# Kernel tuning notes

Hardware: AMD Instinct MI355X
Metric: run time of the kernel (lower is better)

Reference implementation:

```python
import jax, jax.numpy as jnp
import numpy as np

B, L, DM = 16, 1024, 128
DK = DV = 32
HF, HG, HC, HP, HT, HA = 2, 2, 2, 2, 1, 2  # full, log, local, prob, FFT, auto heads
MA = 25          # series_decomp moving average window
WIN = 32         # local attention causal window
EPS = 1e-5
SCALE = float(1.0 / np.sqrt(DK))

_i = np.arange(L)[:, None]
_j = np.arange(L)[None, :]
_d = _i - _j
# log-sparse: attend to self and keys at power-of-two causal distances
LOG_MASK = jnp.asarray((_d == 0) | ((_d > 0) & ((_d & (_d - 1)) == 0)))
LOC_MASK = jnp.asarray((_d >= 0) & (_d < WIN))
# ProbSparse (Informer, factor=5): fixed sample indices, u = U_part
_U = min(int(5 * np.ceil(np.log(L))), L)
PROB_IDX = jnp.asarray(np.random.RandomState(0).randint(0, L, size=(L, _U)))
AUTO_K = int(np.log(L))  # AutoCorrelation factor=1


def _cconv(x, w, b, pad):
    # x [B,L,DM] -> conv over time in NCH layout; pad-left = causal (Conv pad=2 + Chomp1d(2))
    y = jax.lax.conv_general_dilated(x.swapaxes(1, 2), w, (1,), [(pad, 0)],
                                     dimension_numbers=('NCH', 'OIH', 'NCH'))
    return y + b[None, :, None]


def _heads(y, H, d):
    # faithful to torch: .view(B, L, H, d) applied to [B, C, L] conv output (memory reinterpret)
    return y.reshape(y.shape[0], L, H, d)


def _qkv(xq, xk, xv, wq, bq, wk, bk, wv, bv, H):
    Q = _heads(_cconv(xq, wq, bq, 2), H, DK)
    K = _heads(_cconv(xk, wk, bk, 2), H, DK)
    V = _heads(_cconv(xv, wv, bv, 0), H, DV)
    return Q, K, V


def _attn(Q, K, V, mask=None):
    s = jnp.einsum('blhe,bshe->bhls', Q, K) * SCALE
    if mask is not None:
        s = jnp.where(mask, s, -1e9)
    return jnp.einsum('bhls,bshd->blhd', jax.nn.softmax(s, axis=-1), V)


def _prob_attn(Q, K, V):
    q, k, v = Q.swapaxes(1, 2), K.swapaxes(1, 2), V.swapaxes(1, 2)  # [B,H,L,D]
    Ks = k[:, :, PROB_IDX]                                  # [B,H,L,U,D] sampled keys
    qk = jnp.einsum('bhld,bhlud->bhlu', q, Ks)
    M = qk.max(-1) - qk.sum(-1) / L                         # sparsity measure
    top = jax.lax.top_k(M, _U)[1]                           # [B,H,u] active queries
    qr = jnp.take_along_axis(q, top[..., None], axis=2)
    sc = jnp.einsum('bhud,bhsd->bhus', qr, k) * SCALE
    cu = jnp.einsum('bhus,bhsd->bhud', jax.nn.softmax(sc, -1), v)
    ctx = jnp.broadcast_to(v.mean(axis=2, keepdims=True), v.shape)  # lazy queries get mean(V)
    bi = jnp.arange(v.shape[0])[:, None, None]
    hi = jnp.arange(v.shape[1])[None, :, None]
    return ctx.at[bi, hi, top].set(cu).swapaxes(1, 2)


def _auto_corr(Q, K, V):
    q = Q.transpose(0, 2, 3, 1)  # [B,H,E,L]
    k = K.transpose(0, 2, 3, 1)
    v = V.transpose(0, 2, 3, 1)
    corr = jnp.fft.irfft(jnp.fft.rfft(q, axis=-1) * jnp.conj(jnp.fft.rfft(k, axis=-1)), n=L, axis=-1)
    mv = corr.mean(axis=1).mean(axis=1)                     # [B,L] mean over heads+channels
    idx = jax.lax.top_k(mv.mean(axis=0), AUTO_K)[1]         # shared top-k delays
    w = jax.nn.softmax(mv[:, idx], axis=-1)                 # [B,k]
    tt = jnp.arange(L)
    agg = jnp.zeros_like(v)
    for i in range(AUTO_K):
        agg = agg + v[..., (tt + idx[i]) % L] * w[:, i][:, None, None, None]
    return agg.transpose(0, 3, 1, 2)                        # [B,L,H,E]


def _mavg(x, k):
    # replicate-padded moving average (Autoformer series_decomp) via cumsum
    p = (k - 1) // 2
    xp = jnp.concatenate([jnp.repeat(x[:, :1], p, axis=1), x, jnp.repeat(x[:, -1:], p, axis=1)], axis=1)
    cs = jnp.cumsum(xp, axis=1)
    cs = jnp.concatenate([jnp.zeros_like(cs[:, :1]), cs], axis=1)
    return (cs[:, k:] - cs[:, :-k]) / k


def _forward(fl):
    (iq, ik, iv,
     wqf, bqf, wkf, bkf, wvf, bvf,
     wqg, bqg, wkg, bkg, wvg, bvg,
     wql, bql, wkl, bkl, wvl, bvl,
     wqp, bqp, wkp, bkp, wvp, bvp,
     wqa, bqa, wka, bka, wva, bva,
     wfft, bfft, wap, bap, was, bas, wfc) = fl
    ctx = []
    Q, K, V = _qkv(iq, ik, iv, wqf, bqf, wkf, bkf, wvf, bvf, HF)
    ctx.append(_attn(Q, K, V))
    Q, K, V = _qkv(iq, ik, iv, wqg, bqg, wkg, bkg, wvg, bvg, HG)
    ctx.append(_attn(Q, K, V, LOG_MASK))
    Q, K, V = _qkv(iq, ik, iv, wql, bql, wkl, bkl, wvl, bvl, HC)
    ctx.append(_attn(Q, K, V, LOC_MASK))
    Q, K, V = _qkv(iq, ik, iv, wqp, bqp, wkp, bkp, wvp, bvp, HP)
    ctx.append(_prob_attn(Q, K, V))
    cf = jnp.fft.fft(iq, axis=1).real                       # FFT branch
    ctx.append((cf @ wfft + bfft).reshape(B, L, HT, DV))
    Q, K, V = _qkv(iq, ik, iv, wqa, bqa, wka, bka, wva, bva, HA)
    ca = _auto_corr(Q, K, V).reshape(B, L, HA * DV) @ wap + bap
    ca = iq + ca                                            # residual (dropout=eval identity)
    ca = ca - _mavg(ca, MA)                                 # seasonal part of series_decomp
    ctx.append((ca @ was + bas).reshape(B, L, HA, DV))
    c = jnp.concatenate(ctx, axis=2).reshape(B, L, -1)
    out = c @ wfc + iq
    mu = out.mean(-1, keepdims=True)
    var = out.var(-1, keepdims=True)                        # fresh LayerNorm: weight=1, bias=0
    return (out - mu) / jnp.sqrt(var + EPS)


def setup_inputs() -> dict:
    ks = iter(jax.random.split(jax.random.key(0), 64))
    def n(shape, s=0.02):
        return jax.random.normal(next(ks), shape, dtype=jnp.float32) * s
    d = {}
    d['input_Q'] = jax.random.normal(next(ks), (B, L, DM), dtype=jnp.float32)
    d['input_K'] = jax.random.normal(next(ks), (B, L, DM), dtype=jnp.float32)
    d['input_V'] = jax.random.normal(next(ks), (B, L, DM), dtype=jnp.float32)
    for nm, H in [('full', HF), ('log', HG), ('loc', HC), ('prob', HP), ('auto', HA)]:
        d['wq_' + nm] = n((DK * H, DM, 3)); d['bq_' + nm] = n((DK * H,))
        d['wk_' + nm] = n((DK * H, DM, 3)); d['bk_' + nm] = n((DK * H,))
        d['wv_' + nm] = n((DV * H, DM, 1)); d['bv_' + nm] = n((DV * H,))
    d['w_fft'] = n((DM, DV * HT)); d['b_fft'] = n((DV * HT,))
    d['w_aproj'] = n((DV * HA, DM)); d['b_aproj'] = n((DM,))
    d['w_asize'] = n((DM, DV * HA)); d['b_asize'] = n((DV * HA,))
    d['w_fc'] = n(((HF + HG + HC + HP + HT + HA) * DV, DM))
    return d


def reference(input_Q, input_K, input_V, wq_full, bq_full, wk_full, bk_full, wv_full, bv_full, wq_log, bq_log, wk_log, bk_log, wv_log, bv_log, wq_loc, bq_loc, wk_loc, bk_loc, wv_loc, bv_loc, wq_prob, bq_prob, wk_prob, bk_prob, wv_prob, bv_prob, wq_auto, bq_auto, wk_auto, bk_auto, wv_auto, bv_auto, w_fft, b_fft, w_aproj, b_aproj, w_asize, b_asize, w_fc):
    return _forward((input_Q, input_K, input_V, wq_full, bq_full, wk_full, bk_full, wv_full, bv_full, wq_log, bq_log, wk_log, bk_log, wv_log, bv_log, wq_loc, bq_loc, wk_loc, bk_loc, wv_loc, bv_loc, wq_prob, bq_prob, wk_prob, bk_prob, wv_prob, bv_prob, wq_auto, bq_auto, wk_auto, bk_auto, wv_auto, bv_auto, w_fft, b_fft, w_aproj, b_aproj, w_asize, b_asize, w_fc))
```

## Files before the change

### kernel.cpp

```cpp
#include <hip/hip_runtime.h>
#include <hip/hip_bf16.h>
#include <math.h>

#define B_   16
#define L_   1024
#define SCALE_ 0.17677669529663687f

__global__ void mt_kernel(int* __restrict__ pidx) {
  __shared__ unsigned int mt[624];
  int tid = threadIdx.x;
  if (tid == 0) {
    unsigned int s = 0u;
    for (int i = 0; i < 624; ++i) {
      mt[i] = s;
      s = 1812433253u * (s ^ (s >> 30)) + (unsigned)(i + 1);
    }
  }
  __syncthreads();
  const unsigned int HI = 0x80000000u, LO = 0x7fffffffu, MM = 0x9908b0dfu;
  for (int blk = 0; blk < 58; ++blk) {
    unsigned int n0 = 0, n1 = 0, n2 = 0, old623 = 0;
    bool a0 = tid < 227, a2 = tid < 169;
    if (a0) {
      unsigned int y0 = (mt[tid] & HI) | (mt[tid + 1] & LO);
      n0 = mt[tid + 397] ^ (y0 >> 1) ^ ((y0 & 1u) ? MM : 0u);
      unsigned int y1 = (mt[tid + 227] & HI) | (mt[tid + 228] & LO);
      n1 = n0 ^ (y1 >> 1) ^ ((y1 & 1u) ? MM : 0u);
      if (a2) {
        unsigned int y2 = (mt[tid + 454] & HI) | (mt[tid + 455] & LO);
        n2 = n1 ^ (y2 >> 1) ^ ((y2 & 1u) ? MM : 0u);
      }
      if (tid == 169) old623 = mt[623];
    }
    __syncthreads();
    if (a0) {
      mt[tid] = n0;
      mt[tid + 227] = n1;
      if (a2) mt[tid + 454] = n2;
    }
    __syncthreads();
    if (tid == 169) {
      unsigned int y = (old623 & HI) | (mt[0] & LO);
      mt[623] = n1 ^ (y >> 1) ^ ((y & 1u) ? MM : 0u);
    }
    __syncthreads();
    for (int i = tid; i < 624; i += 256) {
      int g = blk * 624 + i;
      if (g < 35840) {
        unsigned int y = mt[i];
        y ^= y >> 11;
        y ^= (y << 7) & 0x9d2c5680u;
        y ^= (y << 15) & 0xefc60000u;
        y ^= y >> 18;
        pidx[g] = (int)(y & 1023u);
      }
    }
  }
}

__device__ __forceinline__ void conv_body(const float* __restrict__ x,
                                          const float* __restrict__ w,
                                          const float* __restrict__ bias,
                                          float* __restrict__ out,
                                          float* smem, int b, int t0, int tid, int is1) {
  int cp = tid & 31;
  int tg = tid >> 5;
  int tt0 = tg * 8;
  float acc0[8], acc1[8];
  float b0v = bias[cp], b1v = bias[cp + 32];
  #pragma unroll
  for (int j = 0; j < 8; ++j) { acc0[j] = b0v; acc1[j] = b1v; }
  if (!is1) {
    float* xs = smem;
    float* ws = smem + 8448;
    for (int i = tid; i < 66 * 128; i += 256) {
      int r = i >> 7, d = i & 127;
      int t = t0 - 2 + r;
      xs[r * 128 + d] = (t >= 0) ? x[(size_t)b * 131072 + (size_t)t * 128 + d] : 0.0f;
    }
    for (int dc = 0; dc < 128; dc += 16) {
      __syncthreads();
      {
        int row = tid >> 2, sub = tid & 3;
        const float* wsrc = w + row * 384 + dc * 3 + sub * 12;
        float* wdst = ws + row * 52 + sub * 12;
        #pragma unroll
        for (int k = 0; k < 12; ++k) wdst[k] = wsrc[k];
      }
      __syncthreads();
      #pragma unroll
      for (int dl = 0; dl < 16; dl += 4) {
        int d0 = dc + dl;
        float4 xr[10];
        #pragma unroll
        for (int r = 0; r < 10; ++r) xr[r] = *(const float4*)&xs[(tt0 + r) * 128 + d0];
        float4 wa0 = *(const float4*)&ws[cp * 52 + dl * 3];
        float4 wa1 = *(const float4*)&ws[cp * 52 + dl * 3 + 4];
        float4 wa2 = *(const float4*)&ws[cp * 52 + dl * 3 + 8];
        float4 wb0 = *(const float4*)&ws[(cp + 32) * 52 + dl * 3];
        float4 wb1 = *(const float4*)&ws[(cp + 32) * 52 + dl * 3 + 4];
        float4 wb2 = *(const float4*)&ws[(cp + 32) * 52 + dl * 3 + 8];
        float w0r[12] = {wa0.x, wa0.y, wa0.z, wa0.w, wa1.x, wa1.y, wa1.z, wa1.w,
                         wa2.x, wa2.y, wa2.z, wa2.w};
        float w1r[12] = {wb0.x, wb0.y, wb0.z, wb0.w, wb1.x, wb1.y, wb1.z, wb1.w,
                         wb2.x, wb2.y, wb2.z, wb2.w};
        #pragma unroll
        for (int j = 0; j < 8; ++j) {
          float a0 = acc0[j], a1 = acc1[j];
          #pragma unroll
          for (int k = 0; k < 3; ++k) {
            float4 xv = xr[j + k];
            a0 = fmaf(w0r[0 + k], xv.x, a0);
            a0 = fmaf(w0r[3 + k], xv.y, a0);
            a0 = fmaf(w0r[6 + k], xv.z, a0);
            a0 = fmaf(w0r[9 + k], xv.w, a0);
            a1 = fmaf(w1r[0 + k], xv.x, a1);
            a1 = fmaf(w1r[3 + k], xv.y, a1);
            a1 = fmaf(w1r[6 + k], xv.z, a1);
            a1 = fmaf(w1r[9 + k], xv.w, a1);
          }
          acc0[j] = a0; acc1[j] = a1;
        }
      }
    }
  } else {
    float* xs = smem;
    float* ws = smem + 8192;
    for (int i = tid; i < 64 * 128; i += 256) {
      int r = i >> 7, d = i & 127;
      xs[r * 128 + d] = x[(size_t)b * 131072 + (size_t)(t0 + r) * 128 + d];
    }
    for (int dc = 0; dc < 128; dc += 32) {
      __syncthreads();
      {
        int row = tid >> 2, sub = tid & 3;
        const float* wsrc = w + row * 128 + dc + sub * 8;
        float* wdst = ws + row * 36 + sub * 8;
        #pragma unroll
        for (int k = 0; k < 8; ++k) wdst[k] = wsrc[k];
      }
      __syncthreads();
      #pragma unroll
      for (int dl = 0; dl < 32; dl += 4) {
        int d0 = dc + dl;
        float4 wv0 = *(const float4*)&ws[cp * 36 + dl];
        float4 wv1 = *(const float4*)&ws[(cp + 32) * 36 + dl];
        #pragma unroll
        for (int j = 0; j < 8; ++j) {
          float4 xv = *(const float4*)&xs[(tt0 + j) * 128 + d0];
          float a0 = acc0[j], a1 = acc1[j];
          a0 = fmaf(wv0.x, xv.x, a0);
          a0 = fmaf(wv0.y, xv.y, a0);
          a0 = fmaf(wv0.z, xv.z, a0);
          a0 = fmaf(wv0.w, xv.w, a0);
          a1 = fmaf(wv1.x, xv.x, a1);
          a1 = fmaf(wv1.y, xv.y, a1);
          a1 = fmaf(wv1.z, xv.z, a1);
          a1 = fmaf(wv1.w, xv.w, a1);
          acc0[j] = a0; acc1[j] = a1;
        }
      }
    }
  }
  float* op0 = out + (size_t)b * 65536 + (size_t)cp * 1024 + t0 + tt0;
  float* op1 = out + (size_t)b * 65536 + (size_t)(cp + 32) * 1024 + t0 + tt0;
  *(float4*)op0 = make_float4(acc0[0], acc0[1], acc0[2], acc0[3]);
  *(float4*)(op0 + 4) = make_float4(acc0[4], acc0[5], acc0[6], acc0[7]);
  *(float4*)op1 = make_float4(acc1[0], acc1[1], acc1[2], acc1[3]);
  *(float4*)(op1 + 4) = make_float4(acc1[4], acc1[5], acc1[6], acc1[7]);
}

__global__ __launch_bounds__(256, 3)
void qkv_conv_kernel(const float* __restrict__ xq, const float* __restrict__ xk,
                     const float* __restrict__ xv,
                     const float* __restrict__ wq, const float* __restrict__ bq,
                     const float* __restrict__ wk, const float* __restrict__ bk,
                     const float* __restrict__ wv, const float* __restrict__ bv,
                     float* __restrict__ qo, float* __restrict__ ko,
                     float* __restrict__ vo) {
  __shared__ float smem[11776];
  int which = blockIdx.z;
  const float* x = (which == 0) ? xq : (which == 1) ? xk : xv;
  const float* w = (which == 0) ? wq : (which == 1) ? wk : wv;
  const float* bias = (which == 0) ? bq : (which == 1) ? bk : bv;
  float* out = (which == 0) ? qo : (which == 1) ? ko : vo;
  conv_body(x, w, bias, out, smem, blockIdx.y, blockIdx.x * 64, threadIdx.x, which == 2);
}

struct ConvArgs {
  const float* x[3];
  const float* w[15];
  const float* bia[15];
  float* outbase;
};
__global__ __launch_bounds__(256, 3)
void qkv_conv_all(ConvArgs a) {
  __shared__ float smem[11776];
  int z = blockIdx.z;
  int which = z % 3;
  float* out = a.outbase + (size_t)z * 1048576;
  conv_body(a.x[which], a.w[z], a.bia[z], out, smem, blockIdx.y, blockIdx.x * 64,
            threadIdx.x, which == 2);
}

__global__ __launch_bounds__(256, 2)
void attn_full_part(const float* __restrict__ Q, const float* __restrict__ K,
                    const float* __restrict__ V, float* __restrict__ part,
                    int stile, int nstage) {
  __shared__ float Ks[128][32];
  __shared__ float Vs[128][32];
  int bh = blockIdx.z, b = bh >> 1, h = bh & 1;
  int l = blockIdx.x * 256 + threadIdx.x;
  int s0 = blockIdx.y * stile;
  const float* Kb = K + (size_t)b * 65536 + h * 32;
  const float* Vb = V + (size_t)b * 65536 + h * 32;
  const float* Qb = Q + (size_t)b * 65536 + h * 32 + (size_t)l * 64;
  float q[32];
  #pragma unroll
  for (int i = 0; i < 8; ++i) {
    float4 v4 = ((const float4*)Qb)[i];
    q[4*i] = v4.x; q[4*i+1] = v4.y; q[4*i+2] = v4.z; q[4*i+3] = v4.w;
  }
  float o[32];
  #pragma unroll
  for (int d = 0; d < 32; ++d) o[d] = 0.0f;
  float ssum = 0.0f;
  for (int st = 0; st < nstage; ++st) {
    __syncthreads();
    int sb = s0 + st * 128;
    for (int i = threadIdx.x; i < 1024; i += 256) {
      int r = i >> 3, d4 = i & 7;
      ((float4*)&Ks[r][0])[d4] = *(const float4*)(Kb + (size_t)(sb + r) * 64 + d4 * 4);
      ((float4*)&Vs[r][0])[d4] = *(const float4*)(Vb + (size_t)(sb + r) * 64 + d4 * 4);
    }
    __syncthreads();
    for (int s = 0; s < 128; s += 2) {
      const float4* kp0 = (const float4*)&Ks[s][0];
      const float4* kp1 = (const float4*)&Ks[s + 1][0];
      float a0 = 0, a1 = 0, a2 = 0, a3 = 0;
      float c0 = 0, c1 = 0, c2 = 0, c3 = 0;
      #pragma unroll
      for (int i = 0; i < 8; ++i) {
        float4 k0 = kp0[i], k1 = kp1[i];
        float qx = q[4*i], qy = q[4*i+1], qz = q[4*i+2], qw = q[4*i+3];
        a0 = fmaf(qx, k0.x, a0); a1 = fmaf(qy, k0.y, a1);
        a2 = fmaf(qz, k0.z, a2); a3 = fmaf(qw, k0.w, a3);
        c0 = fmaf(qx, k1.x, c0); c1 = fmaf(qy, k1.y, c1);
        c2 = fmaf(qz, k1.z, c2); c3 = fmaf(qw, k1.w, c3);
      }
      float p0 = __expf(((a0 + a1) + (a2 + a3)) * SCALE_);
      float p1 = __expf(((c0 + c1) + (c2 + c3)) * SCALE_);
      ssum += p0 + p1;
      const float4* vp0 = (const float4*)&Vs[s][0];
      const float4* vp1 = (const float4*)&Vs[s + 1][0];
      #pragma unroll
      for (int i = 0; i < 8; ++i) {
        float4 v0 = vp0[i], v1 = vp1[i];
        o[4*i]   = fmaf(p0, v0.x, fmaf(p1, v1.x, o[4*i]));
        o[4*i+1] = fmaf(p0, v0.y, fmaf(p1, v1.y, o[4*i+1]));
        o[4*i+2] = fmaf(p0, v0.z, fmaf(p1, v1.z, o[4*i+2]));
        o[4*i+3] = fmaf(p0, v0.w, fmaf(p1, v1.w, o[4*i+3]));
      }
    }
  }
  float* pp = part + (((size_t)bh * gridDim.y + blockIdx.y) * 1024 + l) * 36;
  #pragma unroll
  for (int i = 0; i < 8; ++i)
    ((float4*)pp)[i] = make_float4(o[4*i], o[4*i+1], o[4*i+2], o[4*i+3]);
  pp[32] = ssum;
}

__global__ void attn_full_comb(const float* __restrict__ part, float* __restrict__ cbuf,
                               int nsplit) {
  int idx = blockIdx.x * 128 + threadIdx.x;
  int bh = idx >> 10, l = idx & 1023;
  int b = bh >> 1, h = bh & 1;
  float S = 0.0f;
  float o[32];
  #pragma unroll
  for (int d = 0; d < 32; ++d) o[d] = 0.0f;
  for (int j = 0; j < nsplit; ++j) {
    const float* pp = part + (((size_t)bh * nsplit + j) * 1024 + l) * 36;
    S += pp[32];
    #pragma unroll
    for (int i = 0; i < 8; ++i) {
      float4 v4 = ((const float4*)pp)[i];
      o[4*i] += v4.x; o[4*i+1] += v4.y; o[4*i+2] += v4.z; o[4*i+3] += v4.w;
    }
  }
  float inv = 1.0f / S;
  float* cc = cbuf + ((size_t)b * 1024 + l) * 352 + 0 + h * 32;
  #pragma unroll
  for (int d = 0; d < 32; ++d) cc[d] = o[d] * inv;
}

__global__ void attn_log_kernel(const float* __restrict__ Q, const float* __restrict__ K,
                                const float* __restrict__ V, float* __restrict__ cbuf) {
  int idx = blockIdx.x * 128 + threadIdx.x;
  int bh = idx >> 10, l = idx & 1023;
  int b = bh >> 1, h = bh & 1;
  const float* Qb = Q + (size_t)b * 65536 + h * 32;
  const float* Kb = K + (size_t)b * 65536 + h * 32;
  const float* Vb = V + (size_t)b * 65536 + h * 32;
  float q[32];
  #pragma unroll
  for (int i = 0; i < 8; ++i) {
    float4 v4 = ((const float4*)(Qb + (size_t)l * 64))[i];
    q[4*i] = v4.x; q[4*i+1] = v4.y; q[4*i+2] = v4.z; q[4*i+3] = v4.w;
  }
  float o[32];
  #pragma unroll
  for (int d = 0; d < 32; ++d) o[d] = 0.0f;
  float ssum = 0.0f;
  #pragma unroll
  for (int j = 0; j < 11; ++j) {
    int off = (j == 0) ? 0 : (1 << (j - 1));
    if (off <= l) {
      int s = l - off;
      const float4* kp = (const float4*)(Kb + (size_t)s * 64);
      float a0 = 0, a1 = 0, a2 = 0, a3 = 0;
      #pragma unroll
      for (int i = 0; i < 8; ++i) {
        float4 kv = kp[i];
        a0 = fmaf(q[4*i], kv.x, a0);
        a1 = fmaf(q[4*i+1], kv.y, a1);
        a2 = fmaf(q[4*i+2], kv.z, a2);
        a3 = fmaf(q[4*i+3], kv.w, a3);
      }
      float p = __expf(((a0 + a1) + (a2 + a3)) * SCALE_);
      ssum += p;
      const float4* vp = (const float4*)(Vb + (size_t)s * 64);
      #pragma unroll
      for (int i = 0; i < 8; ++i) {
        float4 vv = vp[i];
        o[4*i]   = fmaf(p, vv.x, o[4*i]);
        o[4*i+1] = fmaf(p, vv.y, o[4*i+1]);
        o[4*i+2] = fmaf(p, vv.z, o[4*i+2]);
        o[4*i+3] = fmaf(p, vv.w, o[4*i+3]);
      }
    }
  }
  float inv = 1.0f / ssum;
  float* cc = cbuf + ((size_t)b * 1024 + l) * 352 + 64 + h * 32;
  #pragma unroll
  for (int d = 0; d < 32; ++d) cc[d] = o[d] * inv;
}

__global__ void attn_loc_kernel(const float* __restrict__ Q, const float* __restrict__ K,
                                const float* __restrict__ V, float* __restrict__ cbuf) {
  int idx = blockIdx.x * 128 + threadIdx.x;
  int bh = idx >> 10, l = idx & 1023;
  int b = bh >> 1, h = bh & 1;
  const float* Qb = Q + (size_t)b * 65536 + h * 32;
  const float* Kb = K + (size_t)b * 65536 + h * 32;
  const float* Vb = V + (size_t)b * 65536 + h * 32;
  float q[32];
  #pragma unroll
  for (int i = 0; i < 8; ++i) {
    float4 v4 = ((const float4*)(Qb + (size_t)l * 64))[i];
    q[4*i] = v4.x; q[4*i+1] = v4.y; q[4*i+2] = v4.z; q[4*i+3] = v4.w;
  }
  float o[32];
  #pragma unroll
  for (int d = 0; d < 32; ++d) o[d] = 0.0f;
  float ssum = 0.0f;
  int jlo = (l >= 31) ? 0 : (31 - l);
  for (int j = jlo; j < 32; ++j) {
    int s = l - 31 + j;
    const float4* kp = (const float4*)(Kb + (size_t)s * 64);
    float a0 = 0, a1 = 0, a2 = 0, a3 = 0;
    #pragma unroll
    for (int i = 0; i < 8; ++i) {
      float4 kv = kp[i];
      a0 = fmaf(q[4*i], kv.x, a0);
      a1 = fmaf(q[4*i+1], kv.y, a1);
      a2 = fmaf(q[4*i+2], kv.z, a2);
      a3 = fmaf(q[4*i+3], kv.w, a3);
    }
    float p = __expf(((a0 + a1) + (a2 + a3)) * SCALE_);
    ssum += p;
    const float4* vp = (const float4*)(Vb + (size_t)s * 64);
    #pragma unroll
    for (int i = 0; i < 8; ++i) {
      float4 vv = vp[i];
      o[4*i]   = fmaf(p, vv.x, o[4*i]);
      o[4*i+1] = fmaf(p, vv.y, o[4*i+1]);
      o[4*i+2] = fmaf(p, vv.z, o[4*i+2]);
      o[4*i+3] = fmaf(p, vv.w, o[4*i+3]);
    }
  }
  float inv = 1.0f / ssum;
  float* cc = cbuf + ((size_t)b * 1024 + l) * 352 + 128 + h * 32;
  #pragma unroll
  for (int d = 0; d < 32; ++d) cc[d] = o[d] * inv;
}

__global__ void prob_m_kernel(const float* __restrict__ Q, const float* __restrict__ K,
                              const int* __restrict__ pidx, float* __restrict__ Mbuf) {
  int idx = blockIdx.x * 128 + threadIdx.x;
  int bh = idx >> 10, l = idx & 1023;
  int b = bh >> 1, h = bh & 1;
  const float* Qb = Q + (size_t)b * 65536 + h * 32;
  const float* Kb = K + (size_t)b * 65536 + h * 32;
  float q[32];
  #pragma unroll
  for (int i = 0; i < 8; ++i) {
    float4 v4 = ((const float4*)(Qb + (size_t)l * 64))[i];
    q[4*i] = v4.x; q[4*i+1] = v4.y; q[4*i+2] = v4.z; q[4*i+3] = v4.w;
  }
  float mx = -1e30f, sm = 0.0f;
  for (int u = 0; u < 35; ++u) {
    int ki = pidx[l * 35 + u];
    const float4* kp = (const float4*)(Kb + (size_t)ki * 64);
    float a0 = 0, a1 = 0, a2 = 0, a3 = 0;
    #pragma unroll
    for (int i = 0; i < 8; ++i) {
      float4 kv = kp[i];
      a0 = fmaf(q[4*i], kv.x, a0);
      a1 = fmaf(q[4*i+1], kv.y, a1);
      a2 = fmaf(q[4*i+2], kv.z, a2);
      a3 = fmaf(q[4*i+3], kv.w, a3);
    }
    float s = (a0 + a1) + (a2 + a3);
    mx = fmaxf(mx, s);
    sm += s;
  }
  Mbuf[(size_t)bh * 1024 + l] = mx - sm * (1.0f / 1024.0f);
}

__global__ void top35_kernel(const float* __restrict__ Mbuf, int* __restrict__ sel) {
  int bh = blockIdx.x;
  int lane = threadIdx.x;
  float v[16];
  const float* Mb = Mbuf + (size_t)bh * 1024 + lane * 16;
  #pragma unroll
  for (int k = 0; k < 16; ++k) v[k] = Mb[k];
  for (int it = 0; it < 35; ++it) {
    float bv = -1e30f; int bi = 0;
    #pragma unroll
    for (int k = 0; k < 16; ++k)
      if (v[k] > bv) { bv = v[k]; bi = k; }
    int gidx = lane * 16 + bi;
    #pragma unroll
    for (int off = 32; off > 0; off >>= 1) {
      float ov = __shfl_down(bv, off, 64);
      int og = __shfl_down(gidx, off, 64);
      if (ov > bv || (ov == bv && og < gidx)) { bv = ov; gidx = og; }
    }
    gidx = __shfl(gidx, 0, 64);
    if (lane == 0) sel[bh * 35 + it] = gidx;
    if ((gidx >> 4) == lane) {
      int kk = gidx & 15;
      #pragma unroll
      for (int k = 0; k < 16; ++k)
        if (k == kk) v[k] = -1e30f;
    }
  }
}

__global__ void prob_fill_kernel(const float* __restrict__ V, float* __restrict__ cbuf) {
  __shared__ float red[256];
  __shared__ float vm[32];
  int bh = blockIdx.x, b = bh >> 1, h = bh & 1;
  int tid = threadIdx.x;
  int d = tid & 31, ch = tid >> 5;
  const float* Vb = V + (size_t)b * 65536 + h * 32;
  float s = 0.0f;
  for (int ss = ch * 128; ss < ch * 128 + 128; ++ss) s += Vb[(size_t)ss * 64 + d];
  red[tid] = s;
  __syncthreads();
  if (ch == 0) {
    float t = 0.0f;
    for (int c = 0; c < 8; ++c) t += red[c * 32 + d];
    vm[d] = t * (1.0f / 1024.0f);
  }
  __syncthreads();
  for (int i = tid; i < 1024 * 32; i += 256) {
    int l = i >> 5, dd = i & 31;
    cbuf[((size_t)b * 1024 + l) * 352 + 192 + h * 32 + dd] = vm[dd];
  }
}

__global__ void prob_part_kernel(const float* __restrict__ Q, const float* __restrict__ K,
                                 const float* __restrict__ V, const int* __restrict__ sel,
                                 float* __restrict__ ppart) {
  int bh = blockIdx.y, b = bh >> 1, h = bh & 1;
  int sc0 = blockIdx.x * 64;
  int u = threadIdx.x;
  int uu = (u < 35) ? u : 34;
  int l = sel[bh * 35 + uu];
  const float* Qb = Q + (size_t)b * 65536 + h * 32;
  const float* Kb = K + (size_t)b * 65536 + h * 32;
  const float* Vb = V + (size_t)b * 65536 + h * 32;
  float q[32];
  #pragma unroll
  for (int i = 0; i < 8; ++i) {
    float4 v4 = ((const float4*)(Qb + (size_t)l * 64))[i];
    q[4*i] = v4.x; q[4*i+1] = v4.y; q[4*i+2] = v4.z; q[4*i+3] = v4.w;
  }
  float o[32];
  #pragma unroll
  for (int dd = 0; dd < 32; ++dd) o[dd] = 0.0f;
  float ssum = 0.0f;
  for (int s = sc0; s < sc0 + 64; ++s) {
    const float4* kp = (const float4*)(Kb + (size_t)s * 64);
    float a0 = 0, a1 = 0, a2 = 0, a3 = 0;
    #pragma unroll
    for (int i = 0; i < 8; ++i) {
      float4 kv = kp[i];
      a0 = fmaf(q[4*i], kv.x, a0);
      a1 = fmaf(q[4*i+1], kv.y, a1);
      a2 = fmaf(q[4*i+2], kv.z, a2);
      a3 = fmaf(q[4*i+3], kv.w, a3);
    }
    float p = __expf(((a0 + a1) + (a2 + a3)) * SCALE_);
    ssum += p;
    const float4* vp = (const float4*)(Vb + (size_t)s * 64);
    #pragma unroll
    for (int i = 0; i < 8; ++i) {
      float4 vv = vp[i];
      o[4*i]   = fmaf(p, vv.x, o[4*i]);
      o[4*i+1] = fmaf(p, vv.y, o[4*i+1]);
      o[4*i+2] = fmaf(p, vv.z, o[4*i+2]);
      o[4*i+3] = fmaf(p, vv.w, o[4*i+3]);
    }
  }
  if (u < 35) {
    float* pp = ppart + (((size_t)bh * 16 + blockIdx.x) * 35 + u) * 36;
    #pragma unroll
    for (int i = 0; i < 8; ++i)
      ((float4*)pp)[i] = make_float4(o[4*i], o[4*i+1], o[4*i+2], o[4*i+3]);
    pp[32] = ssum;
  }
}

__global__ void prob_comb_kernel(const float* __restrict__ ppart, const int* __restrict__ sel,
                                 float* __restrict__ cbuf) {
  int t = blockIdx.x * 64 + threadIdx.x;
  if (t >= 32 * 35) return;
  int bh = t / 35, u = t % 35;
  int b = bh >> 1, h = bh & 1;
  int l = sel[bh * 35 + u];
  float S = 0.0f;
  float o[32];
  #pragma unroll
  for (int d = 0; d < 32; ++d) o[d] = 0.0f;
  for (int j = 0; j < 16; ++j) {
    const float* pp = ppart + (((size_t)bh * 16 + j) * 35 + u) * 36;
    S += pp[32];
    #pragma unroll
    for (int i = 0; i < 8; ++i) {
      float4 v4 = ((const float4*)pp)[i];
      o[4*i] += v4.x; o[4*i+1] += v4.y; o[4*i+2] += v4.z; o[4*i+3] += v4.w;
    }
  }
  float inv = 1.0f / S;
  float* cc = cbuf + ((size_t)b * 1024 + l) * 352 + 192 + h * 32;
  #pragma unroll
  for (int d = 0; d < 32; ++d) cc[d] = o[d] * inv;
}

__global__ void auto_mv_part(const float* __restrict__ Qa, const float* __restrict__ Ka,
                             float* __restrict__ part) {
  __shared__ float qs[1280];
  int c = blockIdx.x, tq = blockIdx.y, b = blockIdx.z;
  int tid = threadIdx.x;
  int tau0 = tq * 256;
  const float* Qb = Qa + (size_t)b * 65536 + (size_t)c * 1024;
  const float* Kb = Ka + (size_t)b * 65536 + (size_t)c * 1024;
  for (int i = tid; i < 1280; i += 256) qs[i] = Qb[(tau0 + i) & 1023];
  __syncthreads();
  float a0 = 0, a1 = 0, a2 = 0, a3 = 0;
  for (int t = 0; t < 1024; t += 8) {
    float4 k0 = *(const float4*)(Kb + t);
    float4 k1 = *(const float4*)(Kb + t + 4);
    const float* qp = &qs[t + tid];
    a0 = fmaf(k0.x, qp[0], a0);
    a1 = fmaf(k0.y, qp[1], a1);
    a2 = fmaf(k0.z, qp[2], a2);
    a3 = fmaf(k0.w, qp[3], a3);
    a0 = fmaf(k1.x, qp[4], a0);
    a1 = fmaf(k1.y, qp[5], a1);
    a2 = fmaf(k1.z, qp[6], a2);
    a3 = fmaf(k1.w, qp[7], a3);
  }
  part[(((size_t)b * 64 + c) << 10) + tau0 + tid] = (a0 + a1) + (a2 + a3);
}

__global__ void auto_mv_reduce(const float* __restrict__ part, float* __restrict__ mv) {
  int idx = blockIdx.x * 256 + threadIdx.x;
  int b = idx >> 10, tau = idx & 1023;
  float s = 0.0f;
  for (int c = 0; c < 64; ++c) s += part[(((size_t)b * 64 + c) << 10) + tau];
  mv[(size_t)b * 1024 + tau] = s * (1.0f / 64.0f);
}

__global__ void auto_top6_kernel(const float* __restrict__ mv, int* __restrict__ idx6,
                                 float* __restrict__ w6) {
  __shared__ int id6s[6];
  int lane = threadIdx.x;
  float v[16];
  #pragma unroll
  for (int k = 0; k < 16; ++k) {
    int i = lane * 16 + k;
    float s = 0.0f;
    for (int b = 0; b < 16; ++b) s += mv[(size_t)b * 1024 + i];
    v[k] = s;
  }
  for (int it = 0; it < 6; ++it) {
    float bv = -1e30f; int bi = 0;
    #pragma unroll
    for (int k = 0; k < 16; ++k)
      if (v[k] > bv) { bv = v[k]; bi = k; }
    int gidx = lane * 16 + bi;
    #pragma unroll
    for (int off = 32; off > 0; off >>= 1) {
      float ov = __shfl_down(bv, off, 64);
      int og = __shfl_down(gidx, off, 64);
      if (ov > bv || (ov == bv && og < gidx)) { bv = ov; gidx = og; }
    }
    gidx = __shfl(gidx, 0, 64);
    if (lane == 0) { idx6[it] = gidx; id6s[it] = gidx; }
    if ((gidx >> 4) == lane) {
      int kk = gidx & 15;
      #pragma unroll
      for (int k = 0; k < 16; ++k)
        if (k == kk) v[k] = -1e30f;
    }
  }
  __syncthreads();
  if (lane < 16) {
    int b = lane;
    float vals[6]; float mx = -1e30f;
    #pragma unroll
    for (int j = 0; j < 6; ++j) { vals[j] = mv[(size_t)b * 1024 + id6s[j]]; mx = fmaxf(mx, vals[j]); }
    float s = 0.0f;
    #pragma unroll
    for (int j = 0; j < 6; ++j) { vals[j] = __expf(vals[j] - mx); s += vals[j]; }
    #pragma unroll
    for (int j = 0; j < 6; ++j) w6[b * 6 + j] = vals[j] / s;
  }
}

__global__ void auto_agg_kernel(const float* __restrict__ Va, const float* __restrict__ iq,
                                const float* __restrict__ wap, const float* __restrict__ bap,
                                const int* __restrict__ idx6, const float* __restrict__ w6,
                                float* __restrict__ ca) {
  __shared__ float aggs[16][64];
  __shared__ float w6s[6];
  __shared__ int id6[6];
  int b = blockIdx.y, t0 = blockIdx.x * 16;
  int tid = threadIdx.x;
  if (tid < 6) { w6s[tid] = w6[b * 6 + tid]; id6[tid] = idx6[tid]; }
  __syncthreads();
  const float* Vb = Va + (size_t)b * 65536;
  for (int i = tid; i < 1024; i += 256) {
    int tl = i >> 6, c = i & 63;
    int t = t0 + tl;
    float s = 0.0f;
    #pragma unroll
    for (int j = 0; j < 6; ++j)
      s += w6s[j] * Vb[(size_t)((t + id6[j]) & 1023) * 64 + c];
    aggs[tl][c] = s;
  }
  __syncthreads();
  int dm = tid & 127, tp = tid >> 7;
  float acc[8];
  #pragma unroll
  for (int r = 0; r < 8; ++r) {
    int t = t0 + tp * 8 + r;
    acc[r] = bap[dm] + iq[((size_t)b * 1024 + t) * 128 + dm];
  }
  for (int c = 0; c < 64; ++c) {
    float wv = wap[c * 128 + dm];
    #pragma unroll
    for (int r = 0; r < 8; ++r) acc[r] += aggs[tp * 8 + r][c] * wv;
  }
  #pragma unroll
  for (int r = 0; r < 8; ++r)
    ca[((size_t)b * 1024 + t0 + tp * 8 + r) * 128 + dm] = acc[r];
}

__global__ void auto_ma_kernel(const float* __restrict__ ca, const float* __restrict__ was,
                               const float* __restrict__ bas, float* __restrict__ cbuf) {
  __shared__ float cas[40][128];
  __shared__ float diff[16][128];
  int b = blockIdx.y, t0 = blockIdx.x * 16;
  int tid = threadIdx.x;
  for (int i = tid; i < 40 * 128; i += 256) {
    int r = i >> 7, d = i & 127;
    int t = t0 - 12 + r;
    t = (t < 0) ? 0 : ((t > 1023) ? 1023 : t);
    cas[r][d] = ca[((size_t)b * 1024 + t) * 128 + d];
  }
  __syncthreads();
  int d = tid & 127, hf = tid >> 7;
  int tl0 = hf * 8;
  float s = 0.0f;
  #pragma unroll
  for (int w = 0; w < 25; ++w) s += cas[tl0 + w][d];
  #pragma unroll
  for (int k = 0; k < 8; ++k) {
    int tl = tl0 + k;
    diff[tl][d] = cas[tl + 12][d] - s * (1.0f / 25.0f);
    if (k < 7) s += cas[tl + 25][d] - cas[tl][d];
  }
  __syncthreads();
  int j = tid & 63, tq = tid >> 6;
  float acc[4];
  #pragma unroll
  for (int r = 0; r < 4; ++r) acc[r] = bas[j];
  for (int dd = 0; dd < 128; ++dd) {
    float wv = was[dd * 64 + j];
    #pragma unroll
    for (int r = 0; r < 4; ++r) acc[r] += diff[tq * 4 + r][dd] * wv;
  }
  #pragma unroll
  for (int r = 0; r < 4; ++r)
    cbuf[((size_t)b * 1024 + t0 + tq * 4 + r) * 352 + 288 + j] = acc[r];
}

__global__ void fftY_kernel(const float* __restrict__ x, const float* __restrict__ wfft,
                            float* __restrict__ Y) {
  __shared__ float xs[64][128];
  __shared__ float ws[32][129];
  int b = blockIdx.y, t0 = blockIdx.x * 64;
  int tid = threadIdx.x;
  for (int i = tid; i < 64 * 128; i += 256) {
    int r = i >> 7, d = i & 127;
    xs[r][d] = x[(size_t)b * 131072 + (size_t)(t0 + r) * 128 + d];
  }
  for (int i = tid; i < 4096; i += 256) {
    int d = i >> 5, j = i & 31;
    ws[j][d] = wfft[i];
  }
  __syncthreads();
  int j = tid & 31, tt0 = (tid >> 5) * 8;
  float acc[8];
  #pragma unroll
  for (int r = 0; r < 8; ++r) acc[r] = 0.0f;
  for (int d0 = 0; d0 < 128; d0 += 4) {
    float w0 = ws[j][d0], w1 = ws[j][d0 + 1], w2 = ws[j][d0 + 2], w3 = ws[j][d0 + 3];
    #pragma unroll
    for (int r = 0; r < 8; ++r) {
      float4 xv = *(const float4*)&xs[tt0 + r][d0];
      float a = acc[r];
      a = fmaf(w0, xv.x, a);
      a = fmaf(w1, xv.y, a);
      a = fmaf(w2, xv.z, a);
      a = fmaf(w3, xv.w, a);
      acc[r] = a;
    }
  }
  #pragma unroll
  for (int r = 0; r < 8; ++r)
    Y[((size_t)b * 1024 + t0 + tt0 + r) * 32 + j] = acc[r];
}

__global__ void fftT_kernel(const float* __restrict__ Y, const float* __restrict__ bfft,
                            float* __restrict__ cbuf) {
  __shared__ float ys[256 * 32];
  __shared__ float altred[8][32];
  int b = blockIdx.y, fbase = blockIdx.x * 64;
  int tid = threadIdx.x;
  int fi = tid & 31, jg = tid >> 5, j0 = jg * 4;
  int f0 = fbase + fi * 2;
  const float TWO_PI_N = 6.283185307179586476925f / 1024.0f;
  float ca0, sa0, ca1, sa1;
  sincosf(TWO_PI_N * (float)f0, &sa0, &ca0);
  sincosf(TWO_PI_N * (float)(f0 + 1), &sa1, &ca1);
  float cr0 = 1.0f, ci0 = 0.0f, cr1 = 1.0f, ci1 = 0.0f;
  float4 acc0 = make_float4(0.f, 0.f, 0.f, 0.f);
  float4 acc1 = make_float4(0.f, 0.f, 0.f, 0.f);
  bool do512 = (blockIdx.x == 0);
  int aj = tid & 31, arow = tid >> 5;
  float alt = 0.0f;
  for (int chk = 0; chk < 4; ++chk) {
    __syncthreads();
    const float4* Yp = (const float4*)(Y + ((size_t)b * 1024 + chk * 256) * 32);
    for (int i = tid; i < 2048; i += 256) ((float4*)ys)[i] = Yp[i];
    __syncthreads();
    for (int tl = 0; tl < 256; ++tl) {
      float4 yv = *(const float4*)&ys[tl * 32 + j0];
      acc0.x = fmaf(cr0, yv.x, acc0.x);
      acc0.y = fmaf(cr0, yv.y, acc0.y);
      acc0.z = fmaf(cr0, yv.z, acc0.z);
      acc0.w = fmaf(cr0, yv.w, acc0.w);
      acc1.x = fmaf(cr1, yv.x, acc1.x);
      acc1.y = fmaf(cr1, yv.y, acc1.y);
      acc1.z = fmaf(cr1, yv.z, acc1.z);
      acc1.w = fmaf(cr1, yv.w, acc1.w);
      float nr0 = cr0 * ca0 - ci0 * sa0;
      float ni0 = cr0 * sa0 + ci0 * ca0;
      cr0 = nr0; ci0 = ni0;
      float nr1 = cr1 * ca1 - ci1 * sa1;
      float ni1 = cr1 * sa1 + ci1 * ca1;
      cr1 = nr1; ci1 = ni1;
    }
    if (do512) {
      int tb = arow * 32;
      #pragma unroll 8
      for (int k = 0; k < 32; ++k) {
        float y = ys[(tb + k) * 32 + aj];
        alt += ((tb + k) & 1) ? -y : y;
      }
    }
  }
  float b0 = bfft[j0], b1 = bfft[j0 + 1], b2 = bfft[j0 + 2], b3 = bfft[j0 + 3];
  float* cc0 = cbuf + ((size_t)b * 1024 + f0) * 352 + 256 + j0;
  cc0[0] = acc0.x + b0; cc0[1] = acc0.y + b1; cc0[2] = acc0.z + b2; cc0[3] = acc0.w + b3;
  float* cc1 = cbuf + ((size_t)b * 1024 + f0 + 1) * 352 + 256 + j0;
  cc1[0] = acc1.x + b0; cc1[1] = acc1.y + b1; cc1[2] = acc1.z + b2; cc1[3] = acc1.w + b3;
  if (f0 > 0) {
    float* cm0 = cbuf + ((size_t)b * 1024 + (1024 - f0)) * 352 + 256 + j0;
    cm0[0] = acc0.x + b0; cm0[1] = acc0.y + b1; cm0[2] = acc0.z + b2; cm0[3] = acc0.w + b3;
  }
  {
    float* cm1 = cbuf + ((size_t)b * 1024 + (1024 - f0 - 1)) * 352 + 256 + j0;
    cm1[0] = acc1.x + b0; cm1[1] = acc1.y + b1; cm1[2] = acc1.z + b2; cm1[3] = acc1.w + b3;
  }
  if (do512) {
    altred[arow][aj] = alt;
    __syncthreads();
    if (tid < 32) {
      float s = 0.0f;
      #pragma unroll
      for (int r = 0; r < 8; ++r) s += altred[r][tid];
      cbuf[((size_t)b * 1024 + 512) * 352 + 256 + tid] = s + bfft[tid];
    }
  }
}

__global__ void fc_ln_kernel(const float* __restrict__ cbuf, const float* __restrict__ wfc,
                             const float* __restrict__ iq, float* __restrict__ out) {
  __shared__ float cs[16][352];
  __shared__ float os[16][128];
  int b = blockIdx.y, t0 = blockIdx.x * 16;
  int tid = threadIdx.x;
  for (int i = tid; i < 16 * 352; i += 256) {
    int r = i / 352, col = i % 352;
    cs[r][col] = cbuf[((size_t)b * 1024 + t0 + r) * 352 + col];
  }
  __syncthreads();
  int j = tid & 127, half = tid >> 7;
  float acc[8];
  #pragma unroll
  for (int k = 0; k < 8; ++k)
    acc[k] = iq[((size_t)b * 1024 + t0 + half * 8 + k) * 128 + j];
  for (int i = 0; i < 352; ++i) {
    float wv = wfc[i * 128 + j];
    #pragma unroll
    for (int k = 0; k < 8; ++k) acc[k] += cs[half * 8 + k][i] * wv;
  }
  #pragma unroll
  for (int k = 0; k < 8; ++k) os[half * 8 + k][j] = acc[k];
  __syncthreads();
  int wid = tid >> 6, lane = tid & 63;
  for (int rr = 0; rr < 4; ++rr) {
    int r = wid * 4 + rr;
    float x0 = os[r][lane], x1 = os[r][lane + 64];
    float s1 = x0 + x1;
    float s2 = x0 * x0 + x1 * x1;
    #pragma unroll
    for (int k = 32; k > 0; k >>= 1) {
      s1 += __shfl_xor(s1, k, 64);
      s2 += __shfl_xor(s2, k, 64);
    }
    float mean = s1 * (1.0f / 128.0f);
    float var = s2 * (1.0f / 128.0f) - mean * mean;
    float rstd = 1.0f / sqrtf(var + 1e-5f);
    float* op = out + ((size_t)b * 1024 + t0 + r) * 128;
    op[lane] = (x0 - mean) * rstd;
    op[lane + 64] = (x1 - mean) * rstd;
  }
}

extern "C" void kernel_launch(void* const* d_in, const int* in_sizes, int n_in,
                              void* d_out, int out_size, void* d_ws, size_t ws_size,
                              hipStream_t stream) {
  (void)in_sizes; (void)n_in; (void)out_size;
  const float* inQ = (const float*)d_in[0];
  const float* inK = (const float*)d_in[1];
  const float* inV = (const float*)d_in[2];
  const float *wq[5], *bq[5], *wk[5], *bk[5], *wv[5], *bv[5];
  for (int br = 0; br < 5; ++br) {
    wq[br] = (const float*)d_in[3 + br * 6 + 0];
    bq[br] = (const float*)d_in[3 + br * 6 + 1];
    wk[br] = (const float*)d_in[3 + br * 6 + 2];
    bk[br] = (const float*)d_in[3 + br * 6 + 3];
    wv[br] = (const float*)d_in[3 + br * 6 + 4];
    bv[br] = (const float*)d_in[3 + br * 6 + 5];
  }
  const float* wfft = (const float*)d_in[33];
  const float* bfft = (const float*)d_in[34];
  const float* wap  = (const float*)d_in[35];
  const float* bap  = (const float*)d_in[36];
  const float* was  = (const float*)d_in[37];
  const float* bas  = (const float*)d_in[38];
  const float* wfc  = (const float*)d_in[39];
  float* out = (float*)d_out;

  bool mega = ws_size >= (size_t)128 * 1024 * 1024;
  int nsplit = (ws_size >= (size_t)76 * 1024 * 1024) ? 8 : 4;
  int stile = 1024 / nsplit;
  int nstage = stile / 128;

  char* wsb = (char*)d_ws;
  size_t off = 0;
  auto alloc = [&](size_t bytes) -> void* {
    void* p = wsb + off;
    off += (bytes + 255) & ~(size_t)255;
    return p;
  };
  int*   pidx = (int*)  alloc((size_t)35840 * 4);
  float* qkvall = (float*)alloc((size_t)(mega ? 15 : 3) * 1048576 * 4);
  float* cbuf = (float*)alloc((size_t)16 * 1024 * 352 * 4);
  float* fpart = (float*)alloc((size_t)32 * nsplit * 1024 * 36 * 4);
  float* Mbuf = (float*)alloc((size_t)32 * 1024 * 4);
  int*   sel  = (int*)  alloc((size_t)32 * 35 * 4);
  float* mvb  = (float*)alloc((size_t)16 * 1024 * 4);
  int*   idx6 = (int*)  alloc(64);
  float* w6   = (float*)alloc((size_t)16 * 6 * 4);
  float* ppart = fpart;
  float* cab   = fpart;
  float* mpart = (float*)((char*)fpart + (size_t)8 * 1024 * 1024);
  float* Ybuf  = (float*)((char*)fpart + (size_t)12 * 1024 * 1024);

  mt_kernel<<<1, 256, 0, stream>>>(pidx);

  if (mega) {
    ConvArgs ca;
    ca.x[0] = inQ; ca.x[1] = inK; ca.x[2] = inV;
    for (int br = 0; br < 5; ++br) {
      ca.w[br * 3 + 0] = wq[br]; ca.bia[br * 3 + 0] = bq[br];
      ca.w[br * 3 + 1] = wk[br]; ca.bia[br * 3 + 1] = bk[br];
      ca.w[br * 3 + 2] = wv[br]; ca.bia[br * 3 + 2] = bv[br];
    }
    ca.outbase = qkvall;
    qkv_conv_all<<<dim3(16, 16, 15), 256, 0, stream>>>(ca);
  }
  auto bufs = [&](int br, float*& qb, float*& kb, float*& vb) {
    int bi = mega ? br : 0;
    qb = qkvall + (size_t)(bi * 3 + 0) * 1048576;
    kb = qkvall + (size_t)(bi * 3 + 1) * 1048576;
    vb = qkvall + (size_t)(bi * 3 + 2) * 1048576;
  };
  auto conv_branch = [&](int br, float* qb, float* kb, float* vb) {
    if (!mega)
      qkv_conv_kernel<<<dim3(16, 16, 3), 256, 0, stream>>>(
          inQ, inK, inV, wq[br], bq[br], wk[br], bk[br], wv[br], bv[br], qb, kb, vb);
  };
  float *qb, *kb, *vb;

  bufs(0, qb, kb, vb);
  conv_branch(0, qb, kb, vb);
  attn_full_part<<<dim3(4, nsplit, 32), 256, 0, stream>>>(qb, kb, vb, fpart, stile, nstage);
  attn_full_comb<<<256, 128, 0, stream>>>(fpart, cbuf, nsplit);

  bufs(1, qb, kb, vb);
  conv_branch(1, qb, kb, vb);
  attn_log_kernel<<<256, 128, 0, stream>>>(qb, kb, vb, cbuf);

  bufs(2, qb, kb, vb);
  conv_branch(2, qb, kb, vb);
  attn_loc_kernel<<<256, 128, 0, stream>>>(qb, kb, vb, cbuf);

  bufs(3, qb, kb, vb);
  conv_branch(3, qb, kb, vb);
  prob_m_kernel<<<256, 128, 0, stream>>>(qb, kb, pidx, Mbuf);
  top35_kernel<<<32, 64, 0, stream>>>(Mbuf, sel);
  prob_fill_kernel<<<32, 256, 0, stream>>>(vb, cbuf);
  prob_part_kernel<<<dim3(16, 32), 64, 0, stream>>>(qb, kb, vb, sel, ppart);
  prob_comb_kernel<<<18, 64, 0, stream>>>(ppart, sel, cbuf);

  bufs(4, qb, kb, vb);
  conv_branch(4, qb, kb, vb);
  auto_mv_part<<<dim3(64, 4, 16), 256, 0, stream>>>(qb, kb, mpart);
  auto_mv_reduce<<<64, 256, 0, stream>>>(mpart, mvb);
  auto_top6_kernel<<<1, 64, 0, stream>>>(mvb, idx6, w6);
  auto_agg_kernel<<<dim3(64, 16), 256, 0, stream>>>(vb, inQ, wap, bap, idx6, w6, cab);
  auto_ma_kernel<<<dim3(64, 16), 256, 0, stream>>>(cab, was, bas, cbuf);

  fftY_kernel<<<dim3(16, 16), 256, 0, stream>>>(inQ, wfft, Ybuf);
  fftT_kernel<<<dim3(8, 16), 256, 0, stream>>>(Ybuf, bfft, cbuf);

  fc_ln_kernel<<<dim3(64, 16), 256, 0, stream>>>(cbuf, wfc, inQ, out);
}
```

Measured before the change: 727.7 us.

## Register-block autocorrelation partial sums: 8 lags per thread with swizzled LDS

The autocorrelation mean-value partial kernel now has each thread compute 8 consecutive lags instead of one. Q values are read from LDS as XOR-swizzled float4s and K loads are reused across the 8 accumulators. This cuts LDS traffic and global K reads per FMA. The grid shrinks from 4096 blocks of 256 threads to 1024 blocks of 128, so the GPU gets far fewer threads and register pressure per thread goes up.

```diff
diff --git a/kernel.cpp b/kernel.cpp
--- a/kernel.cpp
+++ b/kernel.cpp
@@ -562,29 +562,48 @@
 
 __global__ void auto_mv_part(const float* __restrict__ Qa, const float* __restrict__ Ka,
                              float* __restrict__ part) {
-  __shared__ float qs[1280];
-  int c = blockIdx.x, tq = blockIdx.y, b = blockIdx.z;
+  __shared__ float4 qs4[512];
+  int c = blockIdx.x, b = blockIdx.y;
   int tid = threadIdx.x;
-  int tau0 = tq * 256;
   const float* Qb = Qa + (size_t)b * 65536 + (size_t)c * 1024;
   const float* Kb = Ka + (size_t)b * 65536 + (size_t)c * 1024;
-  for (int i = tid; i < 1280; i += 256) qs[i] = Qb[(tau0 + i) & 1023];
-  __syncthreads();
-  float a0 = 0, a1 = 0, a2 = 0, a3 = 0;
+  const float4* Qb4 = (const float4*)Qb;
+  for (int blk = tid; blk < 512; blk += 128) {
+    int pb = blk ^ ((blk >> 3) & 7);
+    qs4[pb] = Qb4[blk & 255];
+  }
+  __syncthreads();
+  float acc[8];
+  #pragma unroll
+  for (int j = 0; j < 8; ++j) acc[j] = 0.0f;
+  int base = 2 * tid;
+  float4 v0, v1;
+  {
+    int b0 = base, b1 = base + 1;
+    v0 = qs4[b0 ^ ((b0 >> 3) & 7)];
+    v1 = qs4[b1 ^ ((b1 >> 3) & 7)];
+  }
   for (int t = 0; t < 1024; t += 8) {
+    int b2 = (t >> 2) + base + 2, b3 = b2 + 1;
+    float4 v2 = qs4[b2 ^ ((b2 >> 3) & 7)];
+    float4 v3 = qs4[b3 ^ ((b3 >> 3) & 7)];
     float4 k0 = *(const float4*)(Kb + t);
     float4 k1 = *(const float4*)(Kb + t + 4);
-    const float* qp = &qs[t + tid];
-    a0 = fmaf(k0.x, qp[0], a0);
-    a1 = fmaf(k0.y, qp[1], a1);
-    a2 = fmaf(k0.z, qp[2], a2);
-    a3 = fmaf(k0.w, qp[3], a3);
-    a0 = fmaf(k1.x, qp[4], a0);
-    a1 = fmaf(k1.y, qp[5], a1);
-    a2 = fmaf(k1.z, qp[6], a2);
-    a3 = fmaf(k1.w, qp[7], a3);
-  }
-  part[(((size_t)b * 64 + c) << 10) + tau0 + tid] = (a0 + a1) + (a2 + a3);
+    float W[16] = {v0.x, v0.y, v0.z, v0.w, v1.x, v1.y, v1.z, v1.w,
+                   v2.x, v2.y, v2.z, v2.w, v3.x, v3.y, v3.z, v3.w};
+    float K8[8] = {k0.x, k0.y, k0.z, k0.w, k1.x, k1.y, k1.z, k1.w};
+    #pragma unroll
+    for (int j = 0; j < 8; ++j) {
+      float a = acc[j];
+      #pragma unroll
+      for (int i = 0; i < 8; ++i) a = fmaf(K8[i], W[j + i], a);
+      acc[j] = a;
+    }
+    v0 = v2; v1 = v3;
+  }
+  float* pp = &part[(((size_t)b * 64 + c) << 10) + tid * 8];
+  *(float4*)pp = make_float4(acc[0], acc[1], acc[2], acc[3]);
+  *(float4*)(pp + 4) = make_float4(acc[4], acc[5], acc[6], acc[7]);
 }
 
 __global__ void auto_mv_reduce(const float* __restrict__ part, float* __restrict__ mv) {
@@ -975,7 +994,7 @@
 
   bufs(4, qb, kb, vb);
   conv_branch(4, qb, kb, vb);
-  auto_mv_part<<<dim3(64, 4, 16), 256, 0, stream>>>(qb, kb, mpart);
+  auto_mv_part<<<dim3(64, 16), 128, 0, stream>>>(qb, kb, mpart);
   auto_mv_reduce<<<64, 256, 0, stream>>>(mpart, mvb);
   auto_top6_kernel<<<1, 64, 0, stream>>>(mvb, idx6, w6);
   auto_agg_kernel<<<dim3(64, 16), 256, 0, stream>>>(vb, inQ, wap, bap, idx6, w6, cab);
```

After: 699.2 us. 3.9% less time.
